# Kernel tuning notes

Hardware: AMD Instinct MI355X
Metric: run time of the kernel (lower is better)

Reference implementation:

```python
import jax, jax.numpy as jnp
import numpy as np

N_TRIPLES = 100_000    # number of (head, rel, attr) triples
TOTAL_CHARS = 1_600_000  # total characters across all attribute strings (~16/triple)
CHAR_VOCAB = 10_000
N_ENT = 100_000
D = 128                # embedding dim shared by char and entity tables


def setup_inputs() -> dict:
    key = jax.random.key(0)
    k1, k2, k3, k4, k5 = jax.random.split(key, 5)
    char_embeddings = jax.random.normal(k1, (CHAR_VOCAB, D), dtype=jnp.float32)
    entity_embeddings = jax.random.normal(k2, (N_ENT, D), dtype=jnp.float32)
    head_ids = jax.random.randint(k3, (N_TRIPLES,), 0, N_ENT, dtype=jnp.int32)
    char_ids = jax.random.randint(k4, (TOTAL_CHARS,), 0, CHAR_VOCAB, dtype=jnp.int32)
    # sorted segment ids emulate the per-triple ragged grouping (offsets form)
    segment_ids = jnp.sort(jax.random.randint(k5, (TOTAL_CHARS,), 0, N_TRIPLES, dtype=jnp.int32))
    return {
        "char_embeddings": char_embeddings,
        "entity_embeddings": entity_embeddings,
        "head_ids": head_ids,
        "char_ids": char_ids,
        "segment_ids": segment_ids,
    }


def reference(char_embeddings, entity_embeddings, head_ids, char_ids, segment_ids):
    n = head_ids.shape[0]
    # ragged embedding-bag: gather char rows, sum within each triple's segment
    t = jax.ops.segment_sum(char_embeddings[char_ids], segment_ids, num_segments=n)  # [N, D]
    h = entity_embeddings[head_ids]  # [N, D]
    # torch.norm with no dim = global Frobenius norm (faithful to original)
    h = h / jnp.linalg.norm(h)
    t = t / jnp.linalg.norm(t)
    return jnp.sum(1.0 - jnp.sum(h * t, axis=1))
```

## Files before the change

kernel.cpp:

```cpp
#include <hip/hip_runtime.h>

#define DIM   128
#define HALF  64
#define CPT   256
#define TAIL  64
#define WPB   4

__global__ __launch_bounds__(256) void fused_kernel(
    const float* __restrict__ char_emb,
    const float* __restrict__ ent,
    const int* __restrict__ head_ids,
    const int* __restrict__ char_ids,
    const int* __restrict__ seg_ids,
    float* __restrict__ pb,
    int total_chars, int n_triples, int hh_per_block)
{
    __shared__ __align__(16) int s_off[WPB][CPT + TAIL];
    __shared__ int s_sid[WPB][CPT + TAIL];
    __shared__ float r_scr[3][WPB];

    const int tid  = threadIdx.x;
    const int lane = tid & 63;
    const int wid  = tid >> 6;
    const int colb = lane << 2;

    float ht = 0.f, tt = 0.f, hh = 0.f;

    const int slice = blockIdx.x & 1;
    const int sco   = slice << 8;
    const int chunk = (blockIdx.x >> 1) * WPB + wid;
    const int start = chunk * CPT;
    const int len   = min(CPT, total_chars - start);
    const int sl    = min(CPT + TAIL, total_chars - start);
    const char* cb  = (const char*)char_emb;
    const float* ee = ent + slice * HALF + lane;

    for (int c = lane; c < sl; c += 64) {
        s_off[wid][c] = (char_ids[start + c] << 9) + sco;
        s_sid[wid][c] = seg_ids[start + c];
    }
    unsigned long long mk[4] = {0ull, 0ull, 0ull, 0ull};
    if (len == CPT) {
#pragma unroll
        for (int grp = 0; grp < 4; ++grp) {
            const int c = start + grp * 64 + lane;
            const int s1 = seg_ids[c];
            const int s0 = (c > 0) ? seg_ids[c - 1] : (s1 + 1);
            mk[grp] = __ballot(s1 != s0);
        }
    }
    __syncthreads();

    if (len == CPT) {
        int cur = __builtin_amdgcn_readfirstlane(s_sid[wid][0]);
        float hv = ee[(size_t)head_ids[cur] * DIM];
        float acc = 0.f;
        bool live = false;
        float vA[16], vB[16];

#define PF(BUF, B) { \
    _Pragma("unroll") \
    for (int q = 0; q < 4; ++q) { \
        const int4 o4 = *(const int4*)&s_off[wid][(B) * 16 + q * 4]; \
        BUF[q * 4 + 0] = *(const float*)(cb + (size_t)(unsigned)(o4.x + colb)); \
        BUF[q * 4 + 1] = *(const float*)(cb + (size_t)(unsigned)(o4.y + colb)); \
        BUF[q * 4 + 2] = *(const float*)(cb + (size_t)(unsigned)(o4.z + colb)); \
        BUF[q * 4 + 3] = *(const float*)(cb + (size_t)(unsigned)(o4.w + colb)); \
    } }

#define CS(BUF, B) { \
    _Pragma("unroll") \
    for (int j = 0; j < 16; ++j) { \
        if (mk[(B) >> 2] & (1ull << (((B) & 3) * 16 + j))) {    \
            if (live) { ht = fmaf(hv, acc, ht); tt = fmaf(acc, acc, tt); } \
            live = true; \
            acc = 0.f; \
            cur = __builtin_amdgcn_readfirstlane(s_sid[wid][(B) * 16 + j]); \
            hv = ee[(size_t)head_ids[cur] * DIM];     \
        } \
        acc += BUF[j]; \
    } }

        PF(vA, 0)
#pragma unroll
        for (int B = 0; B < 16; ++B) {
            if (B + 1 < 16) { if (B & 1) { PF(vA, B + 1) } else { PF(vB, B + 1) } }
            if (B & 1) { CS(vB, B) } else { CS(vA, B) }
        }

        if (live) {
            int e = CPT;
            bool ended = false;
            while (e < sl) {
                const int idx = e + lane;
                const bool differ = (idx < sl) && (s_sid[wid][idx] != cur);
                const unsigned long long bm = __ballot(differ);
                const int run = bm ? (__ffsll((long long)bm) - 1)
                                   : min(64, sl - e);
                for (int j = 0; j < run; j += 4) {
                    const int mm2 = min(4, run - j);
                    float vv[4];
#pragma unroll
                    for (int k = 0; k < 4; ++k) {
                        if (k < mm2)
                            vv[k] = *(const float*)(cb +
                                (size_t)(unsigned)(s_off[wid][e + j + k] + colb));
                    }
                    for (int k = 0; k < mm2; ++k) acc += vv[k];
                }
                e += run;
                if (bm) { ended = true; break; }
            }
            if (!ended && start + sl < total_chars) {
                int gg = start + sl;
                while (gg < total_chars && seg_ids[gg] == cur) {
                    acc += *(const float*)(cb +
                        (size_t)(unsigned)((char_ids[gg] << 9) + sco + colb));
                    ++gg;
                }
            }
            ht = fmaf(hv, acc, ht);
            tt = fmaf(acc, acc, tt);
        }
    } else if (len > 0) {
        const float* cembF = char_emb + slice * HALF + lane;
        int p = 0;
        if (start > 0) {
            const int prev = seg_ids[start - 1];
            while (p < len && seg_ids[start + p] == prev) ++p;
        }
        if (p < len) {
            int cur = seg_ids[start + p];
            float acc = 0.f;
            float hv = ee[(size_t)head_ids[cur] * DIM];
            for (int c = p; c < len; ++c) {
                const int sid = seg_ids[start + c];
                if (sid != cur) {
                    ht += hv * acc; tt += acc * acc;
                    acc = 0.f; cur = sid;
                    hv = ee[(size_t)head_ids[cur] * DIM];
                }
                acc += cembF[(size_t)char_ids[start + c] * DIM];
            }
            int gg = start + len;
            while (gg < total_chars && seg_ids[gg] == cur) {
                acc += cembF[(size_t)char_ids[gg] * DIM];
                ++gg;
            }
            ht += hv * acc; tt += acc * acc;
        }
    }

    {
        const float4* e4 = (const float4*)ent;
        const long base = (long)blockIdx.x * hh_per_block * 32;
        const long lim  = (long)n_triples * 32;
        for (int s = tid; s < hh_per_block * 32; s += 256) {
            const long f = base + s;
            if (f < lim) {
                const int row = (int)(f >> 5);
                const int hid = head_ids[row];
                const float4 v = e4[(size_t)hid * 32 + (int)(f & 31)];
                hh += v.x * v.x + v.y * v.y + v.z * v.z + v.w * v.w;
            }
        }
    }

#pragma unroll
    for (int off = 32; off > 0; off >>= 1) {
        ht += __shfl_down(ht, off);
        tt += __shfl_down(tt, off);
        hh += __shfl_down(hh, off);
    }
    if (lane == 0) { r_scr[0][wid] = ht; r_scr[1][wid] = tt; r_scr[2][wid] = hh; }
    __syncthreads();
    if (tid == 0) {
        float a = 0.f, b = 0.f, c = 0.f;
#pragma unroll
        for (int w = 0; w < WPB; ++w) {
            a += r_scr[0][w]; b += r_scr[1][w]; c += r_scr[2][w];
        }
        pb[blockIdx.x * 3 + 0] = a;
        pb[blockIdx.x * 3 + 1] = b;
        pb[blockIdx.x * 3 + 2] = c;
    }
}

__global__ __launch_bounds__(256) void reduce_kernel(
    const float* __restrict__ pb, int nb, float* __restrict__ out,
    int n_triples)
{
    double ht = 0.0, tt = 0.0, hh = 0.0;
    for (int i = threadIdx.x; i < nb; i += 256) {
        ht += (double)pb[i * 3 + 0];
        tt += (double)pb[i * 3 + 1];
        hh += (double)pb[i * 3 + 2];
    }
#pragma unroll
    for (int off = 32; off > 0; off >>= 1) {
        ht += __shfl_down(ht, off);
        tt += __shfl_down(tt, off);
        hh += __shfl_down(hh, off);
    }
    __shared__ double sd[3][4];
    const int wid = threadIdx.x >> 6;
    if ((threadIdx.x & 63) == 0) { sd[0][wid] = ht; sd[1][wid] = tt; sd[2][wid] = hh; }
    __syncthreads();
    if (threadIdx.x == 0) {
        double a = 0.0, b = 0.0, c = 0.0;
        for (int w = 0; w < 4; ++w) { a += sd[0][w]; b += sd[1][w]; c += sd[2][w]; }
        out[0] = (float)((double)n_triples - a / sqrt(c * b));
    }
}

extern "C" void kernel_launch(void* const* d_in, const int* in_sizes, int n_in,
                              void* d_out, int out_size, void* d_ws, size_t ws_size,
                              hipStream_t stream)
{
    const float* char_emb = (const float*)d_in[0];
    const float* ent_emb  = (const float*)d_in[1];
    const int* head_ids   = (const int*)d_in[2];
    const int* char_ids   = (const int*)d_in[3];
    const int* seg_ids    = (const int*)d_in[4];
    const int n_triples   = in_sizes[2];
    const int total_chars = in_sizes[3];

    const int n_chunks = (total_chars + CPT - 1) / CPT;
    const int bps = (n_chunks + WPB - 1) / WPB;
    const int nsb = 2 * bps;
    const int hhpb = (n_triples + nsb - 1) / nsb;

    float* pb = (float*)d_ws;

    fused_kernel<<<nsb, 256, 0, stream>>>(char_emb, ent_emb, head_ids,
                                          char_ids, seg_ids, pb,
                                          total_chars, n_triples, hhpb);
    reduce_kernel<<<1, 256, 0, stream>>>(pb, nsb, (float*)d_out, n_triples);
}
```

Before: 163.8 us.

## Replace LDS staging of ids with wave-uniform scalar loads and 4-stage ring prefetch

Drops the shared-memory staging of char offsets and segment ids, along with the ballot-built boundary masks and the block barrier. With a wave-uniform start, each wave now reads char_ids and seg_ids directly, which the compiler can turn into scalar loads. It pipelines them through a 4-deep ring of 8-element batches, with id loads two batches ahead of value loads. Segment boundaries are detected by comparing each id to the current segment, and liveness comes from the previous element. The intent is to remove LDS traffic and the sync, at the cost of more global/scalar loads and more register pressure.

```diff
diff --git a/kernel.cpp b/kernel.cpp
--- a/kernel.cpp
+++ b/kernel.cpp
@@ -5,6 +5,8 @@
 #define CPT   256
 #define TAIL  64
 #define WPB   4
+#define BAT   8
+#define NB    (CPT / BAT)
 
 __global__ __launch_bounds__(256) void fused_kernel(
     const float* __restrict__ char_emb,
@@ -15,98 +17,83 @@
     float* __restrict__ pb,
     int total_chars, int n_triples, int hh_per_block)
 {
-    __shared__ __align__(16) int s_off[WPB][CPT + TAIL];
-    __shared__ int s_sid[WPB][CPT + TAIL];
     __shared__ float r_scr[3][WPB];
-
     const int tid  = threadIdx.x;
     const int lane = tid & 63;
     const int wid  = tid >> 6;
-    const int colb = lane << 2;
 
     float ht = 0.f, tt = 0.f, hh = 0.f;
 
     const int slice = blockIdx.x & 1;
-    const int sco   = slice << 8;
     const int chunk = (blockIdx.x >> 1) * WPB + wid;
-    const int start = chunk * CPT;
+    const int start = __builtin_amdgcn_readfirstlane(chunk * CPT);
     const int len   = min(CPT, total_chars - start);
     const int sl    = min(CPT + TAIL, total_chars - start);
-    const char* cb  = (const char*)char_emb;
-    const float* ee = ent + slice * HALF + lane;
-
-    for (int c = lane; c < sl; c += 64) {
-        s_off[wid][c] = (char_ids[start + c] << 9) + sco;
-        s_sid[wid][c] = seg_ids[start + c];
-    }
-    unsigned long long mk[4] = {0ull, 0ull, 0ull, 0ull};
+
+    const float* __restrict__ cbase =
+        (const float*)((const char*)char_emb + (slice << 8));
+    const float* __restrict__ ebase =
+        (const float*)((const char*)ent + (slice << 8));
+
     if (len == CPT) {
-#pragma unroll
-        for (int grp = 0; grp < 4; ++grp) {
-            const int c = start + grp * 64 + lane;
-            const int s1 = seg_ids[c];
-            const int s0 = (c > 0) ? seg_ids[c - 1] : (s1 + 1);
-            mk[grp] = __ballot(s1 != s0);
-        }
-    }
-    __syncthreads();
-
-    if (len == CPT) {
-        int cur = __builtin_amdgcn_readfirstlane(s_sid[wid][0]);
-        float hv = ee[(size_t)head_ids[cur] * DIM];
+        int cur   = seg_ids[start];
+        bool live = (start == 0) || (seg_ids[start - 1] != cur);
+        float hv  = ebase[(size_t)((unsigned)head_ids[cur] * DIM) + lane];
         float acc = 0.f;
-        bool live = false;
-        float vA[16], vB[16];
-
-#define PF(BUF, B) { \
-    _Pragma("unroll") \
-    for (int q = 0; q < 4; ++q) { \
-        const int4 o4 = *(const int4*)&s_off[wid][(B) * 16 + q * 4]; \
-        BUF[q * 4 + 0] = *(const float*)(cb + (size_t)(unsigned)(o4.x + colb)); \
-        BUF[q * 4 + 1] = *(const float*)(cb + (size_t)(unsigned)(o4.y + colb)); \
-        BUF[q * 4 + 2] = *(const float*)(cb + (size_t)(unsigned)(o4.z + colb)); \
-        BUF[q * 4 + 3] = *(const float*)(cb + (size_t)(unsigned)(o4.w + colb)); \
-    } }
-
-#define CS(BUF, B) { \
-    _Pragma("unroll") \
-    for (int j = 0; j < 16; ++j) { \
-        if (mk[(B) >> 2] & (1ull << (((B) & 3) * 16 + j))) {    \
+
+        int   cb_[4][BAT];
+        int   sb_[4][BAT];
+        float vb_[4][BAT];
+
+#define LOADI(BUF, B) { _Pragma("unroll") \
+    for (int j = 0; j < BAT; ++j) { \
+        cb_[BUF][j] = char_ids[start + (B) * BAT + j]; \
+        sb_[BUF][j] = seg_ids[start + (B) * BAT + j]; } }
+
+#define LOADV(BUF) { _Pragma("unroll") \
+    for (int j = 0; j < BAT; ++j) { \
+        vb_[BUF][j] = cbase[((unsigned)cb_[BUF][j] << 7) + lane]; } }
+
+#define CONS(BUF) { _Pragma("unroll") \
+    for (int j = 0; j < BAT; ++j) { \
+        if (sb_[BUF][j] != cur) {               \
             if (live) { ht = fmaf(hv, acc, ht); tt = fmaf(acc, acc, tt); } \
-            live = true; \
-            acc = 0.f; \
-            cur = __builtin_amdgcn_readfirstlane(s_sid[wid][(B) * 16 + j]); \
-            hv = ee[(size_t)head_ids[cur] * DIM];     \
-        } \
-        acc += BUF[j]; \
-    } }
-
-        PF(vA, 0)
-#pragma unroll
-        for (int B = 0; B < 16; ++B) {
-            if (B + 1 < 16) { if (B & 1) { PF(vA, B + 1) } else { PF(vB, B + 1) } }
-            if (B & 1) { CS(vB, B) } else { CS(vA, B) }
-        }
+            live = true; acc = 0.f; cur = sb_[BUF][j]; \
+            hv = ebase[(size_t)((unsigned)head_ids[cur] * DIM) + lane]; } \
+        acc += vb_[BUF][j]; } }
+
+        LOADI(0, 0) LOADI(1, 1)
+        LOADV(0)    LOADV(1)
+#pragma unroll
+        for (int b = 0; b < NB; ++b) {
+            if (b + 2 < NB) LOADI((b + 2) & 3, b + 2)
+            CONS(b & 3)
+            if (b + 2 < NB) LOADV((b + 2) & 3)
+        }
+#undef LOADI
+#undef LOADV
+#undef CONS
 
         if (live) {
             int e = CPT;
             bool ended = false;
             while (e < sl) {
                 const int idx = e + lane;
-                const bool differ = (idx < sl) && (s_sid[wid][idx] != cur);
+                const bool differ = (idx < sl) && (seg_ids[start + idx] != cur);
                 const unsigned long long bm = __ballot(differ);
                 const int run = bm ? (__ffsll((long long)bm) - 1)
                                    : min(64, sl - e);
                 for (int j = 0; j < run; j += 4) {
-                    const int mm2 = min(4, run - j);
+                    const int mm = min(4, run - j);
                     float vv[4];
 #pragma unroll
-                    for (int k = 0; k < 4; ++k) {
-                        if (k < mm2)
-                            vv[k] = *(const float*)(cb +
-                                (size_t)(unsigned)(s_off[wid][e + j + k] + colb));
+                    for (int q = 0; q < 4; ++q) {
+                        if (q < mm) {
+                            const int cid = char_ids[start + e + j + q];
+                            vv[q] = cbase[((unsigned)cid << 7) + lane];
+                        }
                     }
-                    for (int k = 0; k < mm2; ++k) acc += vv[k];
+                    for (int q = 0; q < mm; ++q) acc += vv[q];
                 }
                 e += run;
                 if (bm) { ended = true; break; }
@@ -114,8 +101,7 @@
             if (!ended && start + sl < total_chars) {
                 int gg = start + sl;
                 while (gg < total_chars && seg_ids[gg] == cur) {
-                    acc += *(const float*)(cb +
-                        (size_t)(unsigned)((char_ids[gg] << 9) + sco + colb));
+                    acc += cbase[((unsigned)char_ids[gg] << 7) + lane];
                     ++gg;
                 }
             }
@@ -123,7 +109,6 @@
             tt = fmaf(acc, acc, tt);
         }
     } else if (len > 0) {
-        const float* cembF = char_emb + slice * HALF + lane;
         int p = 0;
         if (start > 0) {
             const int prev = seg_ids[start - 1];
@@ -132,19 +117,19 @@
         if (p < len) {
             int cur = seg_ids[start + p];
             float acc = 0.f;
-            float hv = ee[(size_t)head_ids[cur] * DIM];
+            float hv = ebase[(size_t)((unsigned)head_ids[cur] * DIM) + lane];
             for (int c = p; c < len; ++c) {
                 const int sid = seg_ids[start + c];
                 if (sid != cur) {
                     ht += hv * acc; tt += acc * acc;
                     acc = 0.f; cur = sid;
-                    hv = ee[(size_t)head_ids[cur] * DIM];
+                    hv = ebase[(size_t)((unsigned)head_ids[cur] * DIM) + lane];
                 }
-                acc += cembF[(size_t)char_ids[start + c] * DIM];
+                acc += cbase[((unsigned)char_ids[start + c] << 7) + lane];
             }
             int gg = start + len;
             while (gg < total_chars && seg_ids[gg] == cur) {
-                acc += cembF[(size_t)char_ids[gg] * DIM];
+                acc += cbase[((unsigned)char_ids[gg] << 7) + lane];
                 ++gg;
             }
             ht += hv * acc; tt += acc * acc;
```

New measurement: 187.5 us. 1.14x slower.

## Process full 128-wide rows per wavefront with float2 loads instead of split halves

Applied to the files above, without the earlier changes.

Removes the split of each chunk into two column halves handled by separate blocks. Each lane now loads a float2 so one wavefront covers the whole 512-byte row, which halves the block count and removes the duplicate reads of char_ids, seg_ids and head_ids and the duplicate boundary scans. Entity row loads are marked nontemporal. In exchange, each block does twice the per-thread gather work and holds more registers for the double buffers, and there are fewer blocks to hide latency.

```diff
diff --git a/kernel.cpp b/kernel.cpp
--- a/kernel.cpp
+++ b/kernel.cpp
@@ -1,10 +1,12 @@
 #include <hip/hip_runtime.h>
 
 #define DIM   128
-#define HALF  64
 #define CPT   256
 #define TAIL  64
 #define WPB   4
+
+typedef float vf2 __attribute__((ext_vector_type(2)));
+typedef float vf4 __attribute__((ext_vector_type(4)));
 
 __global__ __launch_bounds__(256) void fused_kernel(
     const float* __restrict__ char_emb,
@@ -22,21 +24,19 @@
     const int tid  = threadIdx.x;
     const int lane = tid & 63;
     const int wid  = tid >> 6;
-    const int colb = lane << 2;
+    const int colb = lane << 3;
 
     float ht = 0.f, tt = 0.f, hh = 0.f;
 
-    const int slice = blockIdx.x & 1;
-    const int sco   = slice << 8;
-    const int chunk = (blockIdx.x >> 1) * WPB + wid;
+    const int chunk = blockIdx.x * WPB + wid;
     const int start = chunk * CPT;
     const int len   = min(CPT, total_chars - start);
     const int sl    = min(CPT + TAIL, total_chars - start);
-    const char* cb  = (const char*)char_emb;
-    const float* ee = ent + slice * HALF + lane;
+    const char* cb  = (const char*)char_emb + colb;
+    const char* eb  = (const char*)ent + colb;
 
     for (int c = lane; c < sl; c += 64) {
-        s_off[wid][c] = (char_ids[start + c] << 9) + sco;
+        s_off[wid][c] = char_ids[start + c] << 9;
         s_sid[wid][c] = seg_ids[start + c];
     }
     unsigned long long mk[4] = {0ull, 0ull, 0ull, 0ull};
@@ -53,32 +53,37 @@
 
     if (len == CPT) {
         int cur = __builtin_amdgcn_readfirstlane(s_sid[wid][0]);
-        float hv = ee[(size_t)head_ids[cur] * DIM];
-        float acc = 0.f;
+        vf2 hv = __builtin_nontemporal_load(
+            (const vf2*)(eb + ((size_t)(unsigned)head_ids[cur] << 9)));
+        vf2 acc = (vf2){0.f, 0.f};
         bool live = false;
-        float vA[16], vB[16];
+        vf2 vA[16], vB[16];
 
 #define PF(BUF, B) { \
     _Pragma("unroll") \
     for (int q = 0; q < 4; ++q) { \
         const int4 o4 = *(const int4*)&s_off[wid][(B) * 16 + q * 4]; \
-        BUF[q * 4 + 0] = *(const float*)(cb + (size_t)(unsigned)(o4.x + colb)); \
-        BUF[q * 4 + 1] = *(const float*)(cb + (size_t)(unsigned)(o4.y + colb)); \
-        BUF[q * 4 + 2] = *(const float*)(cb + (size_t)(unsigned)(o4.z + colb)); \
-        BUF[q * 4 + 3] = *(const float*)(cb + (size_t)(unsigned)(o4.w + colb)); \
+        BUF[q * 4 + 0] = *(const vf2*)(cb + (size_t)(unsigned)o4.x); \
+        BUF[q * 4 + 1] = *(const vf2*)(cb + (size_t)(unsigned)o4.y); \
+        BUF[q * 4 + 2] = *(const vf2*)(cb + (size_t)(unsigned)o4.z); \
+        BUF[q * 4 + 3] = *(const vf2*)(cb + (size_t)(unsigned)o4.w); \
     } }
 
 #define CS(BUF, B) { \
     _Pragma("unroll") \
     for (int j = 0; j < 16; ++j) { \
         if (mk[(B) >> 2] & (1ull << (((B) & 3) * 16 + j))) {    \
-            if (live) { ht = fmaf(hv, acc, ht); tt = fmaf(acc, acc, tt); } \
+            if (live) { \
+                ht = fmaf(hv.x, acc.x, ht); ht = fmaf(hv.y, acc.y, ht); \
+                tt = fmaf(acc.x, acc.x, tt); tt = fmaf(acc.y, acc.y, tt); \
+            } \
             live = true; \
-            acc = 0.f; \
+            acc = (vf2){0.f, 0.f}; \
             cur = __builtin_amdgcn_readfirstlane(s_sid[wid][(B) * 16 + j]); \
-            hv = ee[(size_t)head_ids[cur] * DIM];     \
+            hv = __builtin_nontemporal_load( \
+                (const vf2*)(eb + ((size_t)(unsigned)head_ids[cur] << 9))); \
         } \
-        acc += BUF[j]; \
+        acc.x += BUF[j].x; acc.y += BUF[j].y; \
     } }
 
         PF(vA, 0)
@@ -87,6 +92,8 @@
             if (B + 1 < 16) { if (B & 1) { PF(vA, B + 1) } else { PF(vB, B + 1) } }
             if (B & 1) { CS(vB, B) } else { CS(vA, B) }
         }
+#undef PF
+#undef CS
 
         if (live) {
             int e = CPT;
@@ -99,14 +106,16 @@
                                    : min(64, sl - e);
                 for (int j = 0; j < run; j += 4) {
                     const int mm2 = min(4, run - j);
-                    float vv[4];
+                    vf2 vv[4];
 #pragma unroll
                     for (int k = 0; k < 4; ++k) {
                         if (k < mm2)
-                            vv[k] = *(const float*)(cb +
-                                (size_t)(unsigned)(s_off[wid][e + j + k] + colb));
+                            vv[k] = *(const vf2*)(cb +
+                                (size_t)(unsigned)s_off[wid][e + j + k]);
                     }
-                    for (int k = 0; k < mm2; ++k) acc += vv[k];
+                    for (int k = 0; k < mm2; ++k) {
+                        acc.x += vv[k].x; acc.y += vv[k].y;
+                    }
                 }
                 e += run;
                 if (bm) { ended = true; break; }
@@ -114,16 +123,16 @@
             if (!ended && start + sl < total_chars) {
                 int gg = start + sl;
                 while (gg < total_chars && seg_ids[gg] == cur) {
-                    acc += *(const float*)(cb +
-                        (size_t)(unsigned)((char_ids[gg] << 9) + sco + colb));
+                    const vf2 v = *(const vf2*)(cb +
+                        (size_t)(unsigned)(char_ids[gg] << 9));
+                    acc.x += v.x; acc.y += v.y;
                     ++gg;
                 }
             }
-            ht = fmaf(hv, acc, ht);
-            tt = fmaf(acc, acc, tt);
+            ht = fmaf(hv.x, acc.x, ht); ht = fmaf(hv.y, acc.y, ht);
+            tt = fmaf(acc.x, acc.x, tt); tt = fmaf(acc.y, acc.y, tt);
         }
     } else if (len > 0) {
-        const float* cembF = char_emb + slice * HALF + lane;
         int p = 0;
         if (start > 0) {
             const int prev = seg_ids[start - 1];
@@ -131,36 +140,45 @@
         }
         if (p < len) {
             int cur = seg_ids[start + p];
-            float acc = 0.f;
-            float hv = ee[(size_t)head_ids[cur] * DIM];
+            vf2 acc = (vf2){0.f, 0.f};
+            vf2 hv = __builtin_nontemporal_load(
+                (const vf2*)(eb + ((size_t)(unsigned)head_ids[cur] << 9)));
             for (int c = p; c < len; ++c) {
                 const int sid = seg_ids[start + c];
                 if (sid != cur) {
-                    ht += hv * acc; tt += acc * acc;
-                    acc = 0.f; cur = sid;
-                    hv = ee[(size_t)head_ids[cur] * DIM];
+                    ht += hv.x * acc.x + hv.y * acc.y;
+                    tt += acc.x * acc.x + acc.y * acc.y;
+                    acc = (vf2){0.f, 0.f}; cur = sid;
+                    hv = __builtin_nontemporal_load(
+                        (const vf2*)(eb + ((size_t)(unsigned)head_ids[cur] << 9)));
                 }
-                acc += cembF[(size_t)char_ids[start + c] * DIM];
+                const vf2 v = *(const vf2*)(cb +
+                    (size_t)(unsigned)(char_ids[start + c] << 9));
+                acc.x += v.x; acc.y += v.y;
             }
             int gg = start + len;
             while (gg < total_chars && seg_ids[gg] == cur) {
-                acc += cembF[(size_t)char_ids[gg] * DIM];
+                const vf2 v = *(const vf2*)(cb +
+                    (size_t)(unsigned)(char_ids[gg] << 9));
+                acc.x += v.x; acc.y += v.y;
                 ++gg;
             }
-            ht += hv * acc; tt += acc * acc;
+            ht += hv.x * acc.x + hv.y * acc.y;
+            tt += acc.x * acc.x + acc.y * acc.y;
         }
     }
 
     {
-        const float4* e4 = (const float4*)ent;
+        const vf4* e4 = (const vf4*)ent;
         const long base = (long)blockIdx.x * hh_per_block * 32;
         const long lim  = (long)n_triples * 32;
         for (int s = tid; s < hh_per_block * 32; s += 256) {
-            const long f = base + s;
-            if (f < lim) {
-                const int row = (int)(f >> 5);
+            const long f2 = base + s;
+            if (f2 < lim) {
+                const int row = (int)(f2 >> 5);
                 const int hid = head_ids[row];
-                const float4 v = e4[(size_t)hid * 32 + (int)(f & 31)];
+                const vf4 v = __builtin_nontemporal_load(
+                    e4 + (size_t)hid * 32 + (int)(f2 & 31));
                 hh += v.x * v.x + v.y * v.y + v.z * v.z + v.w * v.w;
             }
         }
@@ -226,8 +244,7 @@
     const int total_chars = in_sizes[3];
 
     const int n_chunks = (total_chars + CPT - 1) / CPT;
-    const int bps = (n_chunks + WPB - 1) / WPB;
-    const int nsb = 2 * bps;
+    const int nsb = (n_chunks + WPB - 1) / WPB;
     const int hhpb = (n_triples + nsb - 1) / nsb;
 
     float* pb = (float*)d_ws;
```

Result: slower. 203.7 us (+24.3%).
